# Kernel tuning notes

Hardware: AMD Instinct MI355X
Metric: run time of the kernel (lower is better)

## Reference

```python
import jax, jax.numpy as jnp
import numpy as np

IN_CH, OUT_CH = 32, 32
MODES1, MODES2 = 16, 16
B, L, H, W = 8, 16, 64, 33


def setup_inputs() -> dict:
    key = jax.random.key(0)
    k = jax.random.split(key, 6)
    scale = 1.0 / (IN_CH * OUT_CH)
    wshape = (IN_CH, OUT_CH, MODES1, MODES2)
    return {
        "x_re": jax.random.normal(k[0], (B, L, IN_CH, H, W), dtype=jnp.float32),
        "x_im": jax.random.normal(k[1], (B, L, IN_CH, H, W), dtype=jnp.float32),
        "w1_re": scale * jax.random.normal(k[2], wshape, dtype=jnp.float32),
        "w1_im": scale * jax.random.normal(k[3], wshape, dtype=jnp.float32),
        "w2_re": scale * jax.random.normal(k[4], wshape, dtype=jnp.float32),
        "w2_im": scale * jax.random.normal(k[5], wshape, dtype=jnp.float32),
    }


def _mul2d(x, w):
    # x: [B, L, C_in, m1, m2] complex; w: [C_in, C_out, m1, m2] complex
    return jnp.einsum("blcij,coij->bloij", x, w)


def reference(x_re, x_im, w1_re, w1_im, w2_re, w2_im):
    x = jax.lax.complex(x_re, x_im)          # [B, L, C, H, W] complex64
    w1 = jax.lax.complex(w1_re, w1_im)       # [C_in, C_out, m1, m2]
    w2 = jax.lax.complex(w2_re, w2_im)
    Bx, Lx, Cx, Hx, Wx = x.shape
    m1 = min(Hx, MODES1)
    m2 = min(Wx, MODES2)

    out = jnp.zeros((Bx, Lx, OUT_CH, Hx, Wx), dtype=x.dtype)
    # low positive frequencies (top-left corner)
    out = out.at[:, :, :, :m1, :m2].set(
        _mul2d(x[:, :, :, :m1, :m2], w1[:, :, :m1, :m2]))
    # low negative frequencies along H (bottom-left corner)
    if Hx > 1 and (Hx > MODES1 or Wx > MODES2):
        out = out.at[:, :, :, -m1:, :m2].set(
            _mul2d(x[:, :, :, -m1:, :m2], w2[:, :, :m1, :m2]))
    # return complex result as trailing real/imag dim (float32)
    return jnp.stack([out.real, out.imag], axis=-1)
```

## Files before the change

kernel.cpp:

```cpp
#include <hip/hip_runtime.h>

#define HW 2112L
typedef float f32x4 __attribute__((ext_vector_type(4)));
typedef short s16x8 __attribute__((ext_vector_type(8)));

#define WT_PLANE 1048576L
#define OFF_WHR 0L
#define OFF_WLR (WT_PLANE)
#define OFF_WHI (2*WT_PLANE)
#define OFF_WLI (3*WT_PLANE)

__device__ __forceinline__ ushort f2bf(float f) {
    unsigned u = __float_as_uint(f);
    u += 0x7FFF + ((u >> 16) & 1);
    return (ushort)(u >> 16);
}
__device__ __forceinline__ void split_bf(float v, ushort& hi, ushort& lo) {
    hi = f2bf(v);
    float hf = __uint_as_float(((unsigned)hi) << 16);
    lo = f2bf(v - hf);
}

__global__ __launch_bounds__(256) void k1_prep_fill(
    const float* __restrict__ w1_re, const float* __restrict__ w1_im,
    const float* __restrict__ w2_re, const float* __restrict__ w2_im,
    float* __restrict__ out, char* __restrict__ ws)
{
    const int tid = threadIdx.x, bid = blockIdx.x;

    if (bid >= 64) {
        const int fid = bid - 64;
        int gtid = fid * 256 + tid, n = 1984 * 256;
        float4* out4 = (float4*)out;
        const float4 z = make_float4(0.f, 0.f, 0.f, 0.f);
        for (int idx = gtid; idx < 4096 * 528; idx += n) {
            int plane = idx / 528;
            int k = idx - plane * 528;
            out4[(long)plane * 1056 + 264 + k] = z;
        }
        return;
    }

    const int r = bid >> 5, i = (bid >> 1) & 15, nt = bid & 1;
    const float* wre = r ? w2_re : w1_re;
    const float* wim = r ? w2_im : w1_im;
    const int col = tid >> 4, j = tid & 15, o = nt * 16 + col;
    const int modeLin = (r * 16 + i) * 16 + j;
    s16x8* phr = (s16x8*)(ws + OFF_WHR);
    s16x8* plr = (s16x8*)(ws + OFF_WLR);
    s16x8* phi = (s16x8*)(ws + OFF_WHI);
    s16x8* pli = (s16x8*)(ws + OFF_WLI);
    #pragma unroll
    for (int kg = 0; kg < 4; ++kg) {
        s16x8 hr, lr, hi2, li2;
        #pragma unroll
        for (int e = 0; e < 8; ++e) {
            int c = kg * 8 + e;
            long src = ((long)(c * 32 + o) * 16 + i) * 16 + j;
            ushort a, b;
            split_bf(wre[src], a, b); hr[e] = (short)a; lr[e] = (short)b;
            split_bf(wim[src], a, b); hi2[e] = (short)a; li2[e] = (short)b;
        }
        long off = (long)(modeLin * 2 + nt) * 64 + kg * 16 + col;
        phr[off] = hr; plr[off] = lr; phi[off] = hi2; pli[off] = li2;
    }
}

__global__ __launch_bounds__(256, 5) void k2_compute(
    const float* __restrict__ x_re, const float* __restrict__ x_im,
    float* __restrict__ out, const char* __restrict__ ws)
{
    const int tid = threadIdx.x, bid = blockIdx.x;
    const int r = bid >> 10, i = (bid >> 6) & 15, bt = (bid >> 1) & 31, jh = bid & 1;
    const int h = r ? 48 + i : i;
    const int bl0 = bt * 4;
    const int modeBase = (r * 16 + i) * 16 + jh * 8;

    __shared__ __align__(16) ushort xfr[8][4][32];
    __shared__ __align__(16) ushort xfi[8][4][32];
    __shared__ __align__(16) float2 stg[128][9];

    const int wave = tid >> 6, lane = tid & 63;
    const int m = lane & 3, ks = lane >> 4, colo = lane & 15;

    const s16x8* Bwhr = (const s16x8*)(ws + OFF_WHR);
    const s16x8* Bwlr = (const s16x8*)(ws + OFF_WLR);
    const s16x8* Bwhi = (const s16x8*)(ws + OFF_WHI);
    const s16x8* Bwli = (const s16x8*)(ws + OFF_WLI);

    s16x8 cBhr[2], cBlr[2], cBhi[2], cBli[2];
    {
        long b0 = ((long)(modeBase + wave * 2) * 2 + 0) * 64 + lane;
        long b1 = ((long)(modeBase + wave * 2) * 2 + 1) * 64 + lane;
        cBhr[0] = Bwhr[b0]; cBlr[0] = Bwlr[b0]; cBhi[0] = Bwhi[b0]; cBli[0] = Bwli[b0];
        cBhr[1] = Bwhr[b1]; cBlr[1] = Bwlr[b1]; cBhi[1] = Bwhi[b1]; cBli[1] = Bwli[b1];
    }

    {
        int jq = tid & 1, c = (tid >> 1) & 31, bl = tid >> 6;
        long base = ((long)((bl0 + bl) * 32 + c)) * HW + h * 33 + jh * 8 + jq * 4;
        f32x4 vr = *(const f32x4*)&x_re[base];
        f32x4 vi = *(const f32x4*)&x_im[base];
        #pragma unroll
        for (int q = 0; q < 4; ++q) {
            xfr[jq * 4 + q][bl][c] = f2bf(vr[q]);
            xfi[jq * 4 + q][bl][c] = f2bf(vi[q]);
        }
    }
    __syncthreads();

    #pragma unroll
    for (int jj = 0; jj < 2; ++jj) {
        const int jl = wave * 2 + jj;

        s16x8 nBhr[2], nBlr[2], nBhi[2], nBli[2];
        if (jj == 0) {
            long b0 = ((long)(modeBase + jl + 1) * 2 + 0) * 64 + lane;
            long b1 = ((long)(modeBase + jl + 1) * 2 + 1) * 64 + lane;
            nBhr[0] = Bwhr[b0]; nBlr[0] = Bwlr[b0]; nBhi[0] = Bwhi[b0]; nBli[0] = Bwli[b0];
            nBhr[1] = Bwhr[b1]; nBlr[1] = Bwlr[b1]; nBhi[1] = Bwhi[b1]; nBli[1] = Bwli[b1];
        }

        s16x8 Ahr = *(const s16x8*)&xfr[jl][m][ks * 8];
        s16x8 Ahi = *(const s16x8*)&xfi[jl][m][ks * 8];

        #pragma unroll
        for (int nt = 0; nt < 2; ++nt) {
            f32x4 accP = (f32x4)0.0f, accN = (f32x4)0.0f, accI = (f32x4)0.0f;
            accP = __builtin_amdgcn_mfma_f32_16x16x32_bf16(Ahr, cBhr[nt], accP, 0, 0, 0);
            accP = __builtin_amdgcn_mfma_f32_16x16x32_bf16(Ahr, cBlr[nt], accP, 0, 0, 0);
            accN = __builtin_amdgcn_mfma_f32_16x16x32_bf16(Ahi, cBhi[nt], accN, 0, 0, 0);
            accN = __builtin_amdgcn_mfma_f32_16x16x32_bf16(Ahi, cBli[nt], accN, 0, 0, 0);
            accI = __builtin_amdgcn_mfma_f32_16x16x32_bf16(Ahr, cBhi[nt], accI, 0, 0, 0);
            accI = __builtin_amdgcn_mfma_f32_16x16x32_bf16(Ahr, cBli[nt], accI, 0, 0, 0);
            accI = __builtin_amdgcn_mfma_f32_16x16x32_bf16(Ahi, cBhr[nt], accI, 0, 0, 0);
            accI = __builtin_amdgcn_mfma_f32_16x16x32_bf16(Ahi, cBlr[nt], accI, 0, 0, 0);

            if (ks == 0) {
                #pragma unroll
                for (int q = 0; q < 4; ++q)
                    stg[q * 32 + nt * 16 + colo][jl] =
                        make_float2(accP[q] - accN[q], accI[q]);
            }
        }

        if (jj == 0) {
            #pragma unroll
            for (int nt = 0; nt < 2; ++nt) {
                cBhr[nt] = nBhr[nt]; cBlr[nt] = nBlr[nt];
                cBhi[nt] = nBhi[nt]; cBli[nt] = nBli[nt];
            }
        }
    }
    __syncthreads();

    float2* out2 = (float2*)out;
    if (jh == 0) {
        #pragma unroll
        for (int p = 0; p < 4; ++p) {
            int idx = p * 256 + tid;
            int row = idx >> 3, w = idx & 7;
            long dst = ((long)(bl0 * 32 + row) * 64 + h) * 33 + w;
            out2[dst] = stg[row][w];
        }
    } else {
        #pragma unroll 2
        for (int t = 0; t < 13; ++t) {
            int idx = t * 256 + tid;
            if (idx < 128 * 25) {
                int row = idx / 25;
                int wl = idx - row * 25;
                float2 v = (wl < 8) ? stg[row][wl] : make_float2(0.f, 0.f);
                long dst = ((long)(bl0 * 32 + row) * 64 + h) * 33 + 8 + wl;
                out2[dst] = v;
            }
        }
    }
}

extern "C" void kernel_launch(void* const* d_in, const int* in_sizes, int n_in,
                              void* d_out, int out_size, void* d_ws, size_t ws_size,
                              hipStream_t stream) {
    const float* x_re  = (const float*)d_in[0];
    const float* x_im  = (const float*)d_in[1];
    const float* w1_re = (const float*)d_in[2];
    const float* w1_im = (const float*)d_in[3];
    const float* w2_re = (const float*)d_in[4];
    const float* w2_im = (const float*)d_in[5];
    float* out = (float*)d_out;
    char* ws = (char*)d_ws;

    k1_prep_fill<<<dim3(2048), dim3(256), 0, stream>>>(
        w1_re, w1_im, w2_re, w2_im, out, ws);
    k2_compute<<<dim3(2048), dim3(256), 0, stream>>>(x_re, x_im, out, ws);
}
```

Measured before the change: 38.98 us.

## Restructure compute kernel to cover all 16 modes per block with two-stage x prefetch

Each compute block now handles all 16 j-modes for one row and processes two batches of 2 (b,l) pairs in sequence, which halves the grid to 1024 blocks. Each wave walks 4 modes instead of 2. While the first stage computes, the x loads for the second stage are issued ahead, and the weight fragments are reloaded between stages. Each block writes full 33-wide output rows, which lets the j-halves share the write path, but the M dimension per MFMA is only half used (m = lane&1) and occupancy drops to 4 blocks.

```diff
diff --git a/kernel.cpp b/kernel.cpp
--- a/kernel.cpp
+++ b/kernel.cpp
@@ -66,115 +66,130 @@
     }
 }
 
-__global__ __launch_bounds__(256, 5) void k2_compute(
+__global__ __launch_bounds__(256, 4) void k2_compute(
     const float* __restrict__ x_re, const float* __restrict__ x_im,
     float* __restrict__ out, const char* __restrict__ ws)
 {
     const int tid = threadIdx.x, bid = blockIdx.x;
-    const int r = bid >> 10, i = (bid >> 6) & 15, bt = (bid >> 1) & 31, jh = bid & 1;
+    const int r = bid >> 9, i = (bid >> 5) & 15, bp = bid & 31;
     const int h = r ? 48 + i : i;
-    const int bl0 = bt * 4;
-    const int modeBase = (r * 16 + i) * 16 + jh * 8;
-
-    __shared__ __align__(16) ushort xfr[8][4][32];
-    __shared__ __align__(16) ushort xfi[8][4][32];
-    __shared__ __align__(16) float2 stg[128][9];
+    const int modeBase = (r * 16 + i) * 16;
+
+    __shared__ __align__(16) ushort xf[2][2][16][2][32];
+    __shared__ __align__(16) float2 stg[64][17];
 
     const int wave = tid >> 6, lane = tid & 63;
-    const int m = lane & 3, ks = lane >> 4, colo = lane & 15;
+    const int m = lane & 1, ks = lane >> 4, colo = lane & 15;
 
     const s16x8* Bwhr = (const s16x8*)(ws + OFF_WHR);
     const s16x8* Bwlr = (const s16x8*)(ws + OFF_WLR);
     const s16x8* Bwhi = (const s16x8*)(ws + OFF_WHI);
     const s16x8* Bwli = (const s16x8*)(ws + OFF_WLI);
 
+    const int sj4 = tid & 3, sc = (tid >> 2) & 31, sbl = tid >> 7;
+
     s16x8 cBhr[2], cBlr[2], cBhi[2], cBli[2];
+
     {
-        long b0 = ((long)(modeBase + wave * 2) * 2 + 0) * 64 + lane;
-        long b1 = ((long)(modeBase + wave * 2) * 2 + 1) * 64 + lane;
+        long b0 = ((long)(modeBase + wave * 4) * 2 + 0) * 64 + lane;
+        long b1 = ((long)(modeBase + wave * 4) * 2 + 1) * 64 + lane;
         cBhr[0] = Bwhr[b0]; cBlr[0] = Bwlr[b0]; cBhi[0] = Bwhi[b0]; cBli[0] = Bwli[b0];
         cBhr[1] = Bwhr[b1]; cBlr[1] = Bwlr[b1]; cBhi[1] = Bwhi[b1]; cBli[1] = Bwli[b1];
     }
 
-    {
-        int jq = tid & 1, c = (tid >> 1) & 31, bl = tid >> 6;
-        long base = ((long)((bl0 + bl) * 32 + c)) * HW + h * 33 + jh * 8 + jq * 4;
-        f32x4 vr = *(const f32x4*)&x_re[base];
-        f32x4 vi = *(const f32x4*)&x_im[base];
+    f32x4 vr1, vi1;
+
+    #pragma unroll 1
+    for (int T = 0; T < 2; ++T) {
+        const int bl0 = bp * 4 + T * 2;
+
+        if (T == 0) {
+            long base = ((long)((bl0 + sbl) * 32 + sc)) * HW + h * 33 + sj4 * 4;
+            f32x4 vr = *(const f32x4*)&x_re[base];
+            f32x4 vi = *(const f32x4*)&x_im[base];
+            #pragma unroll
+            for (int q = 0; q < 4; ++q) {
+                xf[0][0][sj4 * 4 + q][sbl][sc] = f2bf(vr[q]);
+                xf[0][1][sj4 * 4 + q][sbl][sc] = f2bf(vi[q]);
+            }
+            __syncthreads();
+            long base1 = ((long)((bl0 + 2 + sbl) * 32 + sc)) * HW + h * 33 + sj4 * 4;
+            vr1 = *(const f32x4*)&x_re[base1];
+            vi1 = *(const f32x4*)&x_im[base1];
+            __builtin_amdgcn_sched_barrier(0);
+        }
+
         #pragma unroll
-        for (int q = 0; q < 4; ++q) {
-            xfr[jq * 4 + q][bl][c] = f2bf(vr[q]);
-            xfi[jq * 4 + q][bl][c] = f2bf(vi[q]);
-        }
-    }
-    __syncthreads();
-
-    #pragma unroll
-    for (int jj = 0; jj < 2; ++jj) {
-        const int jl = wave * 2 + jj;
-
-        s16x8 nBhr[2], nBlr[2], nBhi[2], nBli[2];
-        if (jj == 0) {
-            long b0 = ((long)(modeBase + jl + 1) * 2 + 0) * 64 + lane;
-            long b1 = ((long)(modeBase + jl + 1) * 2 + 1) * 64 + lane;
-            nBhr[0] = Bwhr[b0]; nBlr[0] = Bwlr[b0]; nBhi[0] = Bwhi[b0]; nBli[0] = Bwli[b0];
-            nBhr[1] = Bwhr[b1]; nBlr[1] = Bwlr[b1]; nBhi[1] = Bwhi[b1]; nBli[1] = Bwli[b1];
-        }
-
-        s16x8 Ahr = *(const s16x8*)&xfr[jl][m][ks * 8];
-        s16x8 Ahi = *(const s16x8*)&xfi[jl][m][ks * 8];
-
-        #pragma unroll
-        for (int nt = 0; nt < 2; ++nt) {
-            f32x4 accP = (f32x4)0.0f, accN = (f32x4)0.0f, accI = (f32x4)0.0f;
-            accP = __builtin_amdgcn_mfma_f32_16x16x32_bf16(Ahr, cBhr[nt], accP, 0, 0, 0);
-            accP = __builtin_amdgcn_mfma_f32_16x16x32_bf16(Ahr, cBlr[nt], accP, 0, 0, 0);
-            accN = __builtin_amdgcn_mfma_f32_16x16x32_bf16(Ahi, cBhi[nt], accN, 0, 0, 0);
-            accN = __builtin_amdgcn_mfma_f32_16x16x32_bf16(Ahi, cBli[nt], accN, 0, 0, 0);
-            accI = __builtin_amdgcn_mfma_f32_16x16x32_bf16(Ahr, cBhi[nt], accI, 0, 0, 0);
-            accI = __builtin_amdgcn_mfma_f32_16x16x32_bf16(Ahr, cBli[nt], accI, 0, 0, 0);
-            accI = __builtin_amdgcn_mfma_f32_16x16x32_bf16(Ahi, cBhr[nt], accI, 0, 0, 0);
-            accI = __builtin_amdgcn_mfma_f32_16x16x32_bf16(Ahi, cBlr[nt], accI, 0, 0, 0);
-
-            if (ks == 0) {
-                #pragma unroll
-                for (int q = 0; q < 4; ++q)
-                    stg[q * 32 + nt * 16 + colo][jl] =
-                        make_float2(accP[q] - accN[q], accI[q]);
-            }
-        }
-
-        if (jj == 0) {
+        for (int jj = 0; jj < 4; ++jj) {
+            const int j = wave * 4 + jj;
+
+            s16x8 nBhr[2], nBlr[2], nBhi[2], nBli[2];
+            if (jj < 3) {
+                long b0 = ((long)(modeBase + j + 1) * 2 + 0) * 64 + lane;
+                long b1 = ((long)(modeBase + j + 1) * 2 + 1) * 64 + lane;
+                nBhr[0] = Bwhr[b0]; nBlr[0] = Bwlr[b0]; nBhi[0] = Bwhi[b0]; nBli[0] = Bwli[b0];
+                nBhr[1] = Bwhr[b1]; nBlr[1] = Bwlr[b1]; nBhi[1] = Bwhi[b1]; nBli[1] = Bwli[b1];
+            }
+
+            s16x8 Ahr = *(const s16x8*)&xf[T][0][j][m][ks * 8];
+            s16x8 Ahi = *(const s16x8*)&xf[T][1][j][m][ks * 8];
+
             #pragma unroll
             for (int nt = 0; nt < 2; ++nt) {
-                cBhr[nt] = nBhr[nt]; cBlr[nt] = nBlr[nt];
-                cBhi[nt] = nBhi[nt]; cBli[nt] = nBli[nt];
-            }
-        }
-    }
-    __syncthreads();
-
-    float2* out2 = (float2*)out;
-    if (jh == 0) {
-        #pragma unroll
-        for (int p = 0; p < 4; ++p) {
-            int idx = p * 256 + tid;
-            int row = idx >> 3, w = idx & 7;
-            long dst = ((long)(bl0 * 32 + row) * 64 + h) * 33 + w;
-            out2[dst] = stg[row][w];
-        }
-    } else {
+                f32x4 accP = (f32x4)0.0f, accN = (f32x4)0.0f, accI = (f32x4)0.0f;
+                accP = __builtin_amdgcn_mfma_f32_16x16x32_bf16(Ahr, cBhr[nt], accP, 0, 0, 0);
+                accP = __builtin_amdgcn_mfma_f32_16x16x32_bf16(Ahr, cBlr[nt], accP, 0, 0, 0);
+                accN = __builtin_amdgcn_mfma_f32_16x16x32_bf16(Ahi, cBhi[nt], accN, 0, 0, 0);
+                accN = __builtin_amdgcn_mfma_f32_16x16x32_bf16(Ahi, cBli[nt], accN, 0, 0, 0);
+                accI = __builtin_amdgcn_mfma_f32_16x16x32_bf16(Ahr, cBhi[nt], accI, 0, 0, 0);
+                accI = __builtin_amdgcn_mfma_f32_16x16x32_bf16(Ahr, cBli[nt], accI, 0, 0, 0);
+                accI = __builtin_amdgcn_mfma_f32_16x16x32_bf16(Ahi, cBhr[nt], accI, 0, 0, 0);
+                accI = __builtin_amdgcn_mfma_f32_16x16x32_bf16(Ahi, cBlr[nt], accI, 0, 0, 0);
+
+                if (ks == 0) {
+                    #pragma unroll
+                    for (int q = 0; q < 2; ++q)
+                        stg[q * 32 + nt * 16 + colo][j] =
+                            make_float2(accP[q] - accN[q], accI[q]);
+                }
+            }
+
+            if (jj < 3) {
+                #pragma unroll
+                for (int nt = 0; nt < 2; ++nt) {
+                    cBhr[nt] = nBhr[nt]; cBlr[nt] = nBlr[nt];
+                    cBhi[nt] = nBhi[nt]; cBli[nt] = nBli[nt];
+                }
+            }
+        }
+        __syncthreads();
+
+        if (T == 0) {
+            #pragma unroll
+            for (int q = 0; q < 4; ++q) {
+                xf[1][0][sj4 * 4 + q][sbl][sc] = f2bf(vr1[q]);
+                xf[1][1][sj4 * 4 + q][sbl][sc] = f2bf(vi1[q]);
+            }
+            long b0 = ((long)(modeBase + wave * 4) * 2 + 0) * 64 + lane;
+            long b1 = ((long)(modeBase + wave * 4) * 2 + 1) * 64 + lane;
+            cBhr[0] = Bwhr[b0]; cBlr[0] = Bwlr[b0]; cBhi[0] = Bwhi[b0]; cBli[0] = Bwli[b0];
+            cBhr[1] = Bwhr[b1]; cBlr[1] = Bwlr[b1]; cBhi[1] = Bwhi[b1]; cBli[1] = Bwli[b1];
+        }
+
+        float2* out2 = (float2*)out;
         #pragma unroll 2
-        for (int t = 0; t < 13; ++t) {
+        for (int t = 0; t < 9; ++t) {
             int idx = t * 256 + tid;
-            if (idx < 128 * 25) {
-                int row = idx / 25;
-                int wl = idx - row * 25;
-                float2 v = (wl < 8) ? stg[row][wl] : make_float2(0.f, 0.f);
-                long dst = ((long)(bl0 * 32 + row) * 64 + h) * 33 + 8 + wl;
+            if (idx < 64 * 33) {
+                int row = idx / 33;
+                int k = idx - row * 33;
+                int bl = row >> 5, o = row & 31;
+                float2 v = (k < 16) ? stg[row][k] : make_float2(0.f, 0.f);
+                long dst = ((long)((bl0 + bl) * 32 + o) * 64 + h) * 33 + k;
                 out2[dst] = v;
             }
         }
+        if (T == 0) __syncthreads();
     }
 }
 
@@ -192,5 +207,5 @@
 
     k1_prep_fill<<<dim3(2048), dim3(256), 0, stream>>>(
         w1_re, w1_im, w2_re, w2_im, out, ws);
-    k2_compute<<<dim3(2048), dim3(256), 0, stream>>>(x_re, x_im, out, ws);
-}
+    k2_compute<<<dim3(1024), dim3(256), 0, stream>>>(x_re, x_im, out, ws);
+}
```

Result: slower. 57.38 us (+47.2%).
